# Kernel tuning notes

Measured on AMD Instinct MI355X. Metric: run time of the kernel, lower is better.

Reference implementation:

```python
import jax, jax.numpy as jnp
import numpy as np

EPS = 1e-6
B, N, K = 4, 65536, 16
D_IN, D_OUT, DH = 8, 16, 8  # DH = d_out // 2


def _bn(x, g, b):
    # train-mode BatchNorm2d over (B, N, K) per channel (channels-last here)
    m = jnp.mean(x, axis=(0, 1, 2))
    v = jnp.var(x, axis=(0, 1, 2))
    return (x - m) * jax.lax.rsqrt(v + EPS) * g + b


def _conv(x, w, b):
    # 1x1 Conv2d == per-point linear; x: (B,N,K,Cin), w: (Cout,Cin)
    return jnp.einsum('bnki,oi->bnko', x, w) + b


def _lse(coords, feats, idx, w, b, g, bt):
    # coords: (B,N,3), feats: (B,N,1,D), idx: (B,N,K)
    nbrs = jnp.take_along_axis(coords[:, :, None, :], idx[:, :, :, None], axis=1)  # (B,N,K,3)
    ctr = jnp.broadcast_to(coords[:, :, None, :], nbrs.shape)
    dist = jnp.ones(idx.shape + (1,), dtype=coords.dtype)  # torch path passes idx only -> dist = ones
    enc = jnp.concatenate([ctr, nbrs, ctr - nbrs, dist], axis=-1)  # (B,N,K,10)
    h = jax.nn.relu(_bn(_conv(enc, w, b), g, bt))
    f = jnp.broadcast_to(feats, idx.shape + (feats.shape[-1],))
    return jnp.concatenate([h, f], axis=-1)  # (B,N,K,2*D)


def _pool(x, sw, w, b, g, bt):
    # attentive pooling: softmax over neighbor axis K (axis=2)
    scores = jax.nn.softmax(jnp.einsum('bnki,oi->bnko', x, sw), axis=2)
    agg = jnp.sum(scores * x, axis=2, keepdims=True)  # (B,N,1,C)
    return jax.nn.relu(_bn(_conv(agg, w, b), g, bt))


def setup_inputs() -> dict:
    key = jax.random.key(0)
    ks = jax.random.split(key, 16)
    rn = lambda k, s: (0.1 * jax.random.normal(k, s)).astype(jnp.float32)
    inp = {
        'coords': jax.random.normal(ks[0], (B, N, 3), dtype=jnp.float32),
        'features': jax.random.normal(ks[1], (B, D_IN, N, 1), dtype=jnp.float32),
        'idx': jax.random.randint(ks[2], (B, N, K), 0, N, dtype=jnp.int32),
        # mlp1: d_in -> d_out//2, no bn, LeakyReLU(0.2)
        'w1': rn(ks[3], (DH, D_IN)), 'b1': jnp.zeros((DH,), jnp.float32),
        # lse1 mlp: 10 -> d_out//2, bn + ReLU
        'lse1_w': rn(ks[4], (DH, 10)), 'lse1_b': jnp.zeros((DH,), jnp.float32),
        'lse1_g': jnp.ones((DH,), jnp.float32), 'lse1_bt': jnp.zeros((DH,), jnp.float32),
        # pool1: in d_out -> out d_out//2
        'p1_sw': rn(ks[5], (D_OUT, D_OUT)),
        'p1_w': rn(ks[6], (DH, D_OUT)), 'p1_b': jnp.zeros((DH,), jnp.float32),
        'p1_g': jnp.ones((DH,), jnp.float32), 'p1_bt': jnp.zeros((DH,), jnp.float32),
        # lse2
        'lse2_w': rn(ks[7], (DH, 10)), 'lse2_b': jnp.zeros((DH,), jnp.float32),
        'lse2_g': jnp.ones((DH,), jnp.float32), 'lse2_bt': jnp.zeros((DH,), jnp.float32),
        # pool2: in d_out -> out d_out
        'p2_sw': rn(ks[8], (D_OUT, D_OUT)),
        'p2_w': rn(ks[9], (D_OUT, D_OUT)), 'p2_b': jnp.zeros((D_OUT,), jnp.float32),
        'p2_g': jnp.ones((D_OUT,), jnp.float32), 'p2_bt': jnp.zeros((D_OUT,), jnp.float32),
        # mlp2: d_out -> 2*d_out (no bn/act)
        'w2': rn(ks[10], (2 * D_OUT, D_OUT)), 'b2': jnp.zeros((2 * D_OUT,), jnp.float32),
        # shortcut: d_in -> 2*d_out, bn, no act
        'sc_w': rn(ks[11], (2 * D_OUT, D_IN)), 'sc_b': jnp.zeros((2 * D_OUT,), jnp.float32),
        'sc_g': jnp.ones((2 * D_OUT,), jnp.float32), 'sc_bt': jnp.zeros((2 * D_OUT,), jnp.float32),
    }
    return inp


def reference(coords, features, idx, w1, b1, lse1_w, lse1_b, lse1_g, lse1_bt,
              p1_sw, p1_w, p1_b, p1_g, p1_bt, lse2_w, lse2_b, lse2_g, lse2_bt,
              p2_sw, p2_w, p2_b, p2_g, p2_bt, w2, b2, sc_w, sc_b, sc_g, sc_bt):
    feats = jnp.transpose(features, (0, 2, 3, 1))  # (B,N,1,d_in) channels-last
    x = jax.nn.leaky_relu(_conv(feats, w1, b1), 0.2)           # (B,N,1,DH)
    x = _lse(coords, x, idx, lse1_w, lse1_b, lse1_g, lse1_bt)  # (B,N,K,D_OUT)
    x = _pool(x, p1_sw, p1_w, p1_b, p1_g, p1_bt)               # (B,N,1,DH)
    x = _lse(coords, x, idx, lse2_w, lse2_b, lse2_g, lse2_bt)  # (B,N,K,D_OUT)
    x = _pool(x, p2_sw, p2_w, p2_b, p2_g, p2_bt)               # (B,N,1,D_OUT)
    out = jax.nn.leaky_relu(
        _conv(x, w2, b2) + _bn(_conv(feats, sc_w, sc_b), sc_g, sc_bt), 0.01)
    return jnp.transpose(out, (0, 3, 1, 2))  # (B, 2*d_out, N, 1)
```

## Files before the change

kernel.cpp:

```cpp
#include <hip/hip_runtime.h>

#define NB 4
#define NN 65536
#define NK 16
#define NP (NB * NN)
#define BN_EPS 1e-6f
#define LOG2E 1.44269504088896f

#define WS_ENC_M   0
#define WS_SC_M    32
#define WS_S_Y2    96
#define WS_SS_Y2   104
#define WS_S_Y4    112
#define WS_SS_Y4   128
#define WS_Y2      1024
#define WS_Y4      (1024 + NP * 8)
#define WS_C4      (1024 + NP * 24)

template <int NCH>
__device__ inline void blockReduceAtomic(float (&v)[NCH], float* __restrict__ dst) {
    __shared__ float red[4][NCH];
    const int lane = threadIdx.x & 63;
    const int wv = threadIdx.x >> 6;
    __syncthreads();
#pragma unroll
    for (int c = 0; c < NCH; c++) {
        float x = v[c];
#pragma unroll
        for (int off = 32; off > 0; off >>= 1) x += __shfl_xor(x, off, 64);
        if (lane == 0) red[wv][c] = x;
    }
    __syncthreads();
    for (int c = threadIdx.x; c < NCH; c += 256)
        atomicAdd(dst + c, red[0][c] + red[1][c] + red[2][c] + red[3][c]);
    __syncthreads();
}

__device__ inline void bn_from_enc(const float* __restrict__ M, const float* __restrict__ w,
                                   float b, float g, float bt, float& sc, float& sh) {
    float u[6];
    u[0] = w[0] + w[6]; u[1] = w[1] + w[7]; u[2] = w[2] + w[8];
    u[3] = w[3] - w[6]; u[4] = w[4] - w[7]; u[5] = w[5] - w[8];
    const float beta = b + w[9];
    float lin = 0.f;
#pragma unroll
    for (int i = 0; i < 6; i++) lin += u[i] * M[i];
    float quad = u[0] * u[0] * M[6] + 2.f * u[0] * u[1] * M[7] + 2.f * u[0] * u[2] * M[8]
               + u[1] * u[1] * M[9] + 2.f * u[1] * u[2] * M[10] + u[2] * u[2] * M[11];
#pragma unroll
    for (int i = 0; i < 3; i++)
#pragma unroll
        for (int j = 0; j < 3; j++) quad += 2.f * u[i] * u[3 + j] * M[12 + i * 3 + j];
    quad += u[3] * u[3] * M[21] + 2.f * u[3] * u[4] * M[22] + 2.f * u[3] * u[5] * M[23]
          + u[4] * u[4] * M[24] + 2.f * u[4] * u[5] * M[25] + u[5] * u[5] * M[26];
    const float cnt = (float)NP * (float)NK;
    const float sum = lin + cnt * beta;
    const float ss = quad + 2.f * beta * lin + cnt * beta * beta;
    const float m = sum / cnt, v = ss / cnt - m * m;
    sc = g * rsqrtf(v + BN_EPS);
    sh = bt - m * sc;
}

__global__ __launch_bounds__(256) void k_stats(
    const float* __restrict__ coords, const float* __restrict__ feats,
    const int* __restrict__ idx, float4* __restrict__ c4, float* __restrict__ ws) {
    const int tid = threadIdx.x;
    const int p = blockIdx.x * 256 + tid;
    const int b = p >> 16;
    const int n = p & (NN - 1);

    {
        float accf[44];
        float f[8];
#pragma unroll
        for (int i = 0; i < 8; i++) f[i] = feats[(b * 8 + i) * NN + n];
#pragma unroll
        for (int i = 0; i < 8; i++) accf[i] = f[i];
        int t2 = 8;
#pragma unroll
        for (int i = 0; i < 8; i++)
#pragma unroll
            for (int j = i; j < 8; j++) accf[t2++] = f[i] * f[j];
        blockReduceAtomic<44>(accf, ws + WS_SC_M);
    }

    const float cx = coords[3 * p], cy = coords[3 * p + 1], cz = coords[3 * p + 2];
    c4[p] = make_float4(cx, cy, cz, 0.f);
    const float* cb = coords + b * NN * 3;
    const int4* ip = (const int4*)idx + p * 4;
    float sn0 = 0.f, sn1 = 0.f, sn2 = 0.f;
    float m00 = 0.f, m01 = 0.f, m02 = 0.f, m11 = 0.f, m12 = 0.f, m22 = 0.f;

    auto proc = [&](float nx, float ny, float nz) {
        sn0 += nx; sn1 += ny; sn2 += nz;
        m00 += nx * nx; m01 += nx * ny; m02 += nx * nz;
        m11 += ny * ny; m12 += ny * nz; m22 += nz * nz;
    };

    int4 v0 = ip[0];
    float ax[4], ay[4], az[4];
    {
        int jj[4] = {v0.x, v0.y, v0.z, v0.w};
#pragma unroll
        for (int e = 0; e < 4; e++) {
            ax[e] = cb[3 * jj[e]]; ay[e] = cb[3 * jj[e] + 1]; az[e] = cb[3 * jj[e] + 2];
        }
    }
#pragma unroll 1
    for (int q = 0; q < 3; q++) {
        const int4 vn = ip[q + 1];
        int jj[4] = {vn.x, vn.y, vn.z, vn.w};
        float tx[4], ty[4], tz[4];
#pragma unroll
        for (int e = 0; e < 4; e++) {
            tx[e] = cb[3 * jj[e]]; ty[e] = cb[3 * jj[e] + 1]; tz[e] = cb[3 * jj[e] + 2];
        }
#pragma unroll
        for (int e = 0; e < 4; e++) proc(ax[e], ay[e], az[e]);
#pragma unroll
        for (int e = 0; e < 4; e++) { ax[e] = tx[e]; ay[e] = ty[e]; az[e] = tz[e]; }
    }
#pragma unroll
    for (int e = 0; e < 4; e++) proc(ax[e], ay[e], az[e]);

    float acc[27];
    acc[0] = 16.f * cx; acc[1] = 16.f * cy; acc[2] = 16.f * cz;
    acc[3] = sn0; acc[4] = sn1; acc[5] = sn2;
    acc[6] = 16.f * cx * cx; acc[7] = 16.f * cx * cy; acc[8] = 16.f * cx * cz;
    acc[9] = 16.f * cy * cy; acc[10] = 16.f * cy * cz; acc[11] = 16.f * cz * cz;
    acc[12] = cx * sn0; acc[13] = cx * sn1; acc[14] = cx * sn2;
    acc[15] = cy * sn0; acc[16] = cy * sn1; acc[17] = cy * sn2;
    acc[18] = cz * sn0; acc[19] = cz * sn1; acc[20] = cz * sn2;
    acc[21] = m00; acc[22] = m01; acc[23] = m02;
    acc[24] = m11; acc[25] = m12; acc[26] = m22;
    blockReduceAtomic<27>(acc, ws + WS_ENC_M);
}

__global__ __launch_bounds__(256) void k_pool1(
    const float4* __restrict__ c4, const float* __restrict__ feats,
    const int* __restrict__ idx,
    const float* __restrict__ w1, const float* __restrict__ b1,
    const float* __restrict__ lse1_w, const float* __restrict__ lse1_b,
    const float* __restrict__ lse1_g, const float* __restrict__ lse1_bt,
    const float* __restrict__ lse2_w, const float* __restrict__ lse2_b,
    const float* __restrict__ lse2_g, const float* __restrict__ lse2_bt,
    const float* __restrict__ p1_sw, const float* __restrict__ p1_w,
    const float* __restrict__ p1_b,
    const float* __restrict__ p2_sw, const float* __restrict__ p2_w,
    const float* __restrict__ p2_b, float* __restrict__ ws) {
    __shared__ float an1[24], dcA[24], dkA[8], an2[24], dcB[24], dkB[8],
        sws1[64], sws2[64], pws1[128], pws2[256], pbs1[8], pbs2[16], w1s[64], b1s[8];
    const int tid = threadIdx.x;
    if (tid < 8) {
        const int c = tid;
        {
            const float* w = lse1_w + c * 10;
            float sc, sh;
            bn_from_enc(ws + WS_ENC_M, w, lse1_b[c], lse1_g[c], lse1_bt[c], sc, sh);
#pragma unroll
            for (int i = 0; i < 3; i++) {
                an1[c * 3 + i] = sc * (w[3 + i] - w[6 + i]);
                dcA[c * 3 + i] = sc * (w[i] + w[6 + i]);
            }
            dkA[c] = sc * (lse1_b[c] + w[9]) + sh;
        }
        {
            const float* w = lse2_w + c * 10;
            float sc, sh;
            bn_from_enc(ws + WS_ENC_M, w, lse2_b[c], lse2_g[c], lse2_bt[c], sc, sh);
#pragma unroll
            for (int i = 0; i < 3; i++) {
                an2[c * 3 + i] = sc * (w[3 + i] - w[6 + i]);
                dcB[c * 3 + i] = sc * (w[i] + w[6 + i]);
            }
            dkB[c] = sc * (lse2_b[c] + w[9]) + sh;
        }
        b1s[c] = b1[c]; pbs1[c] = p1_b[c];
    }
    if (tid < 16) pbs2[tid] = p2_b[tid];
    if (tid < 64) {
        w1s[tid] = w1[tid];
        sws1[tid] = p1_sw[(tid >> 3) * 16 + (tid & 7)] * LOG2E;
        sws2[tid] = p2_sw[(tid >> 3) * 16 + (tid & 7)] * LOG2E;
    }
    if (tid < 128) pws1[tid] = p1_w[tid];
    if (tid < 256) pws2[tid] = p2_w[tid];
    __syncthreads();

    const int p = blockIdx.x * 256 + tid;
    const int b = p >> 16;
    const int n = p & (NN - 1);
    const int boff = b << 16;
    const float4 me = c4[p];
    float d1[8], d2[8];
#pragma unroll
    for (int c = 0; c < 8; c++) {
        d1[c] = dcA[c * 3] * me.x + dcA[c * 3 + 1] * me.y + dcA[c * 3 + 2] * me.z + dkA[c];
        d2[c] = dcB[c * 3] * me.x + dcB[c * 3 + 1] * me.y + dcB[c * 3 + 2] * me.z + dkB[c];
    }
    const int4* ip = (const int4*)idx + p * 4;
    float l1[8] = {}, a1[8] = {}, l2[8] = {}, a2[8] = {};

    auto proc = [&](const float4 nn) {
        float h[8];
#pragma unroll
        for (int c = 0; c < 8; c++) {
            float y = an1[c * 3] * nn.x + an1[c * 3 + 1] * nn.y + an1[c * 3 + 2] * nn.z + d1[c];
            h[c] = y > 0.f ? y : 0.f;
        }
#pragma unroll
        for (int o = 0; o < 8; o++) {
            float s = 0.f;
#pragma unroll
            for (int i = 0; i < 8; i++) s += h[i] * sws1[o * 8 + i];
            float e2 = exp2f(s);
            l1[o] += e2; a1[o] += e2 * h[o];
        }
#pragma unroll
        for (int c = 0; c < 8; c++) {
            float y = an2[c * 3] * nn.x + an2[c * 3 + 1] * nn.y + an2[c * 3 + 2] * nn.z + d2[c];
            h[c] = y > 0.f ? y : 0.f;
        }
#pragma unroll
        for (int o = 0; o < 8; o++) {
            float s = 0.f;
#pragma unroll
            for (int i = 0; i < 8; i++) s += h[i] * sws2[o * 8 + i];
            float e2 = exp2f(s);
            l2[o] += e2; a2[o] += e2 * h[o];
        }
    };

    int4 v = ip[0];
    float4 n0 = c4[boff + v.x], n1 = c4[boff + v.y], n2 = c4[boff + v.z], n3 = c4[boff + v.w];
#pragma unroll 1
    for (int q = 0; q < 3; q++) {
        const int4 vn = ip[q + 1];
        const float4 t0 = c4[boff + vn.x], t1 = c4[boff + vn.y],
                     t2 = c4[boff + vn.z], t3 = c4[boff + vn.w];
        proc(n0); proc(n1); proc(n2); proc(n3);
        n0 = t0; n1 = t1; n2 = t2; n3 = t3;
    }
    proc(n0); proc(n1); proc(n2); proc(n3);

    float f[8];
#pragma unroll
    for (int i = 0; i < 8; i++) f[i] = feats[(b * 8 + i) * NN + n];
    float agg[16];
#pragma unroll
    for (int o = 0; o < 8; o++) agg[o] = a1[o] * __builtin_amdgcn_rcpf(l1[o]);
#pragma unroll
    for (int jq = 0; jq < 8; jq++) {
        float y = b1s[jq];
#pragma unroll
        for (int i = 0; i < 8; i++) y += f[i] * w1s[jq * 8 + i];
        agg[8 + jq] = y > 0.f ? y : 0.2f * y;
    }
    float st[16];
#pragma unroll
    for (int c = 0; c < 8; c++) {
        float y = pbs1[c];
#pragma unroll
        for (int o = 0; o < 16; o++) y += agg[o] * pws1[c * 16 + o];
        ws[WS_Y2 + c * NP + p] = y;
        st[c] = y; st[8 + c] = y * y;
    }
    float g2[8];
#pragma unroll
    for (int o = 0; o < 8; o++) g2[o] = a2[o] * __builtin_amdgcn_rcpf(l2[o]);
#pragma unroll
    for (int c = 0; c < 16; c++) {
        float y = pbs2[c];
#pragma unroll
        for (int o = 0; o < 8; o++) y += g2[o] * pws2[c * 16 + o];
        ws[WS_Y4 + c * NP + p] = y;
    }
    blockReduceAtomic<16>(st, ws + WS_S_Y2);
}

__global__ __launch_bounds__(256) void k_pool2e(
    const float* __restrict__ p1_g, const float* __restrict__ p1_bt,
    const float* __restrict__ p2_w, float* __restrict__ ws) {
    __shared__ float p1sc[8], p1sh[8], pwsb[128];
    const int tid = threadIdx.x;
    if (tid < 8) {
        const int c = tid;
        const float cP = 1.f / (float)NP;
        float m = ws[WS_S_Y2 + c] * cP, vv = ws[WS_SS_Y2 + c] * cP - m * m;
        float sc = p1_g[c] * rsqrtf(vv + BN_EPS);
        p1sc[c] = sc; p1sh[c] = p1_bt[c] - m * sc;
    }
    if (tid < 128) pwsb[tid] = p2_w[(tid >> 3) * 16 + 8 + (tid & 7)];
    __syncthreads();

    const int p = blockIdx.x * 256 + tid;
    float x2[8];
#pragma unroll
    for (int c = 0; c < 8; c++) {
        float y = ws[WS_Y2 + c * NP + p] * p1sc[c] + p1sh[c];
        x2[c] = y > 0.f ? y : 0.f;
    }
    float st[32];
#pragma unroll
    for (int c = 0; c < 16; c++) {
        float y = ws[WS_Y4 + c * NP + p];
#pragma unroll
        for (int o = 0; o < 8; o++) y += x2[o] * pwsb[c * 8 + o];
        ws[WS_Y4 + c * NP + p] = y;
        st[c] = y; st[16 + c] = y * y;
    }
    blockReduceAtomic<32>(st, ws + WS_S_Y4);
}

__global__ __launch_bounds__(256) void k_final(
    const float* __restrict__ feats, const float* __restrict__ w2,
    const float* __restrict__ b2, const float* __restrict__ sc_w,
    const float* __restrict__ sc_b, const float* __restrict__ p2_g,
    const float* __restrict__ p2_bt, const float* __restrict__ sc_g,
    const float* __restrict__ sc_bt, const float* __restrict__ ws,
    float* __restrict__ out) {
    __shared__ float w2s[512], b2s[32], scws[256], scbs[32],
        p2sc[16], p2sh[16], scsc[32], scsh[32];
    const int tid = threadIdx.x;
    for (int i = tid; i < 512; i += 256) w2s[i] = w2[i];
    if (tid < 256) scws[tid] = sc_w[tid];
    if (tid < 32) {
        b2s[tid] = b2[tid]; scbs[tid] = sc_b[tid];
        const int c = tid;
        const float* w = sc_w + c * 8;
        const float* S = ws + WS_SC_M;
        float lin = 0.f;
#pragma unroll
        for (int i = 0; i < 8; i++) lin += w[i] * S[i];
        float quad = 0.f;
        int t2 = 0;
#pragma unroll
        for (int i = 0; i < 8; i++)
#pragma unroll
            for (int j = i; j < 8; j++) {
                const float mm = S[8 + t2++];
                quad += (i == j ? 1.f : 2.f) * w[i] * w[j] * mm;
            }
        const float cnt = (float)NP;
        const float bb = sc_b[c];
        const float sum = lin + cnt * bb;
        const float ss = quad + 2.f * bb * lin + cnt * bb * bb;
        const float m = sum / cnt, vv = ss / cnt - m * m;
        const float sc = sc_g[c] * rsqrtf(vv + BN_EPS);
        scsc[c] = sc; scsh[c] = sc_bt[c] - m * sc;
    }
    if (tid < 16) {
        const int c = tid;
        const float cP = 1.f / (float)NP;
        float m = ws[WS_S_Y4 + c] * cP, vv = ws[WS_SS_Y4 + c] * cP - m * m;
        float sc = p2_g[c] * rsqrtf(vv + BN_EPS);
        p2sc[c] = sc; p2sh[c] = p2_bt[c] - m * sc;
    }
    __syncthreads();

    const int p = blockIdx.x * 256 + tid;
    const int b = p >> 16;
    const int n = p & (NN - 1);
    float x4[16];
#pragma unroll
    for (int c = 0; c < 16; c++) {
        float y = ws[WS_Y4 + c * NP + p] * p2sc[c] + p2sh[c];
        x4[c] = y > 0.f ? y : 0.f;
    }
    float f[8];
#pragma unroll
    for (int i = 0; i < 8; i++) f[i] = feats[(b * 8 + i) * NN + n];
#pragma unroll
    for (int c = 0; c < 32; c++) {
        float s = scbs[c];
#pragma unroll
        for (int i = 0; i < 8; i++) s += f[i] * scws[c * 8 + i];
        s = s * scsc[c] + scsh[c];
        float m = b2s[c];
#pragma unroll
        for (int o = 0; o < 16; o++) m += x4[o] * w2s[c * 16 + o];
        float vv = m + s;
        out[(b * 32 + c) * NN + n] = vv > 0.f ? vv : 0.01f * vv;
    }
}

extern "C" void kernel_launch(void* const* d_in, const int* in_sizes, int n_in,
                              void* d_out, int out_size, void* d_ws, size_t ws_size,
                              hipStream_t stream) {
    (void)in_sizes; (void)n_in; (void)out_size; (void)ws_size;
    const float* coords = (const float*)d_in[0];
    const float* features = (const float*)d_in[1];
    const int* idx = (const int*)d_in[2];
    const float* w1 = (const float*)d_in[3];
    const float* b1 = (const float*)d_in[4];
    const float* lse1_w = (const float*)d_in[5];
    const float* lse1_b = (const float*)d_in[6];
    const float* lse1_g = (const float*)d_in[7];
    const float* lse1_bt = (const float*)d_in[8];
    const float* p1_sw = (const float*)d_in[9];
    const float* p1_w = (const float*)d_in[10];
    const float* p1_b = (const float*)d_in[11];
    const float* p1_g = (const float*)d_in[12];
    const float* p1_bt = (const float*)d_in[13];
    const float* lse2_w = (const float*)d_in[14];
    const float* lse2_b = (const float*)d_in[15];
    const float* lse2_g = (const float*)d_in[16];
    const float* lse2_bt = (const float*)d_in[17];
    const float* p2_sw = (const float*)d_in[18];
    const float* p2_w = (const float*)d_in[19];
    const float* p2_b = (const float*)d_in[20];
    const float* p2_g = (const float*)d_in[21];
    const float* p2_bt = (const float*)d_in[22];
    const float* w2 = (const float*)d_in[23];
    const float* b2 = (const float*)d_in[24];
    const float* sc_w = (const float*)d_in[25];
    const float* sc_b = (const float*)d_in[26];
    const float* sc_g = (const float*)d_in[27];
    const float* sc_bt = (const float*)d_in[28];
    float* ws = (float*)d_ws;
    float* out = (float*)d_out;
    float4* c4 = (float4*)(ws + WS_C4);

    const int NBLK = NP / 256;
    (void)hipMemsetAsync(ws, 0, 144 * sizeof(float), stream);
    k_stats<<<NBLK, 256, 0, stream>>>(coords, features, idx, c4, ws);
    k_pool1<<<NBLK, 256, 0, stream>>>(c4, features, idx, w1, b1,
                                      lse1_w, lse1_b, lse1_g, lse1_bt,
                                      lse2_w, lse2_b, lse2_g, lse2_bt,
                                      p1_sw, p1_w, p1_b, p2_sw, p2_w, p2_b, ws);
    k_pool2e<<<NBLK, 256, 0, stream>>>(p1_g, p1_bt, p2_w, ws);
    k_final<<<NBLK, 256, 0, stream>>>(features, w2, b2, sc_w, sc_b, p2_g, p2_bt,
                                      sc_g, sc_bt, ws, out);
}
```

Measured before the change: 335.9 us.

## Materialize gathered neighbor coords in k_stats and stream them in k_pool1

Splits the old stats kernel into a pack kernel (float4 coords plus feature stats) and a stats kernel that gathers neighbors from the packed float4 array. The stats kernel also writes the gathered neighbor coordinates to a coalesced SoA workspace buffer, so k_pool1 reads them with contiguous loads instead of repeating the random idx-based gather. This trades a second random gather for writing and reading about 48 floats per point (roughly 50 MB each way), and adds one kernel launch.

```diff
diff --git a/kernel.cpp b/kernel.cpp
--- a/kernel.cpp
+++ b/kernel.cpp
@@ -16,6 +16,7 @@
 #define WS_Y2      1024
 #define WS_Y4      (1024 + NP * 8)
 #define WS_C4      (1024 + NP * 24)
+#define WS_NB      (1024 + NP * 28)
 
 template <int NCH>
 __device__ inline void blockReduceAtomic(float (&v)[NCH], float* __restrict__ dst) {
@@ -61,76 +62,71 @@
     sh = bt - m * sc;
 }
 
-__global__ __launch_bounds__(256) void k_stats(
+__global__ __launch_bounds__(256) void k_pack(
     const float* __restrict__ coords, const float* __restrict__ feats,
-    const int* __restrict__ idx, float4* __restrict__ c4, float* __restrict__ ws) {
+    float4* __restrict__ c4, float* __restrict__ ws) {
     const int tid = threadIdx.x;
     const int p = blockIdx.x * 256 + tid;
     const int b = p >> 16;
     const int n = p & (NN - 1);
-
-    {
-        float accf[44];
-        float f[8];
-#pragma unroll
-        for (int i = 0; i < 8; i++) f[i] = feats[(b * 8 + i) * NN + n];
-#pragma unroll
-        for (int i = 0; i < 8; i++) accf[i] = f[i];
-        int t2 = 8;
-#pragma unroll
-        for (int i = 0; i < 8; i++)
-#pragma unroll
-            for (int j = i; j < 8; j++) accf[t2++] = f[i] * f[j];
-        blockReduceAtomic<44>(accf, ws + WS_SC_M);
-    }
-
-    const float cx = coords[3 * p], cy = coords[3 * p + 1], cz = coords[3 * p + 2];
-    c4[p] = make_float4(cx, cy, cz, 0.f);
-    const float* cb = coords + b * NN * 3;
+    c4[p] = make_float4(coords[3 * p], coords[3 * p + 1], coords[3 * p + 2], 0.f);
+    float accf[44];
+    float f[8];
+#pragma unroll
+    for (int i = 0; i < 8; i++) f[i] = feats[(b * 8 + i) * NN + n];
+#pragma unroll
+    for (int i = 0; i < 8; i++) accf[i] = f[i];
+    int t2 = 8;
+#pragma unroll
+    for (int i = 0; i < 8; i++)
+#pragma unroll
+        for (int j = i; j < 8; j++) accf[t2++] = f[i] * f[j];
+    blockReduceAtomic<44>(accf, ws + WS_SC_M);
+}
+
+__global__ __launch_bounds__(256) void k_stats(
+    const float4* __restrict__ c4, const int* __restrict__ idx,
+    float* __restrict__ ws) {
+    const int tid = threadIdx.x;
+    const int p = blockIdx.x * 256 + tid;
+    const int b = p >> 16;
+    const int boff = b << 16;
+    float* __restrict__ nbp = ws + WS_NB;
     const int4* ip = (const int4*)idx + p * 4;
+    const float4 me = c4[p];
+
     float sn0 = 0.f, sn1 = 0.f, sn2 = 0.f;
     float m00 = 0.f, m01 = 0.f, m02 = 0.f, m11 = 0.f, m12 = 0.f, m22 = 0.f;
 
-    auto proc = [&](float nx, float ny, float nz) {
-        sn0 += nx; sn1 += ny; sn2 += nz;
-        m00 += nx * nx; m01 += nx * ny; m02 += nx * nz;
-        m11 += ny * ny; m12 += ny * nz; m22 += nz * nz;
+    auto emit = [&](int k, const float4 nn) {
+        nbp[(3 * k    ) * NP + p] = nn.x;
+        nbp[(3 * k + 1) * NP + p] = nn.y;
+        nbp[(3 * k + 2) * NP + p] = nn.z;
+        sn0 += nn.x; sn1 += nn.y; sn2 += nn.z;
+        m00 += nn.x * nn.x; m01 += nn.x * nn.y; m02 += nn.x * nn.z;
+        m11 += nn.y * nn.y; m12 += nn.y * nn.z; m22 += nn.z * nn.z;
     };
 
-    int4 v0 = ip[0];
-    float ax[4], ay[4], az[4];
-    {
-        int jj[4] = {v0.x, v0.y, v0.z, v0.w};
-#pragma unroll
-        for (int e = 0; e < 4; e++) {
-            ax[e] = cb[3 * jj[e]]; ay[e] = cb[3 * jj[e] + 1]; az[e] = cb[3 * jj[e] + 2];
-        }
-    }
+    int4 v = ip[0];
+    float4 n0 = c4[boff + v.x], n1 = c4[boff + v.y], n2 = c4[boff + v.z], n3 = c4[boff + v.w];
 #pragma unroll 1
     for (int q = 0; q < 3; q++) {
         const int4 vn = ip[q + 1];
-        int jj[4] = {vn.x, vn.y, vn.z, vn.w};
-        float tx[4], ty[4], tz[4];
-#pragma unroll
-        for (int e = 0; e < 4; e++) {
-            tx[e] = cb[3 * jj[e]]; ty[e] = cb[3 * jj[e] + 1]; tz[e] = cb[3 * jj[e] + 2];
-        }
-#pragma unroll
-        for (int e = 0; e < 4; e++) proc(ax[e], ay[e], az[e]);
-#pragma unroll
-        for (int e = 0; e < 4; e++) { ax[e] = tx[e]; ay[e] = ty[e]; az[e] = tz[e]; }
-    }
-#pragma unroll
-    for (int e = 0; e < 4; e++) proc(ax[e], ay[e], az[e]);
+        const float4 t0 = c4[boff + vn.x], t1 = c4[boff + vn.y],
+                     t2 = c4[boff + vn.z], t3 = c4[boff + vn.w];
+        emit(4 * q, n0); emit(4 * q + 1, n1); emit(4 * q + 2, n2); emit(4 * q + 3, n3);
+        n0 = t0; n1 = t1; n2 = t2; n3 = t3;
+    }
+    emit(12, n0); emit(13, n1); emit(14, n2); emit(15, n3);
 
     float acc[27];
-    acc[0] = 16.f * cx; acc[1] = 16.f * cy; acc[2] = 16.f * cz;
+    acc[0] = 16.f * me.x; acc[1] = 16.f * me.y; acc[2] = 16.f * me.z;
     acc[3] = sn0; acc[4] = sn1; acc[5] = sn2;
-    acc[6] = 16.f * cx * cx; acc[7] = 16.f * cx * cy; acc[8] = 16.f * cx * cz;
-    acc[9] = 16.f * cy * cy; acc[10] = 16.f * cy * cz; acc[11] = 16.f * cz * cz;
-    acc[12] = cx * sn0; acc[13] = cx * sn1; acc[14] = cx * sn2;
-    acc[15] = cy * sn0; acc[16] = cy * sn1; acc[17] = cy * sn2;
-    acc[18] = cz * sn0; acc[19] = cz * sn1; acc[20] = cz * sn2;
+    acc[6] = 16.f * me.x * me.x; acc[7] = 16.f * me.x * me.y; acc[8] = 16.f * me.x * me.z;
+    acc[9] = 16.f * me.y * me.y; acc[10] = 16.f * me.y * me.z; acc[11] = 16.f * me.z * me.z;
+    acc[12] = me.x * sn0; acc[13] = me.x * sn1; acc[14] = me.x * sn2;
+    acc[15] = me.y * sn0; acc[16] = me.y * sn1; acc[17] = me.y * sn2;
+    acc[18] = me.z * sn0; acc[19] = me.z * sn1; acc[20] = me.z * sn2;
     acc[21] = m00; acc[22] = m01; acc[23] = m02;
     acc[24] = m11; acc[25] = m12; acc[26] = m22;
     blockReduceAtomic<27>(acc, ws + WS_ENC_M);
@@ -138,7 +134,6 @@
 
 __global__ __launch_bounds__(256) void k_pool1(
     const float4* __restrict__ c4, const float* __restrict__ feats,
-    const int* __restrict__ idx,
     const float* __restrict__ w1, const float* __restrict__ b1,
     const float* __restrict__ lse1_w, const float* __restrict__ lse1_b,
     const float* __restrict__ lse1_g, const float* __restrict__ lse1_bt,
@@ -190,7 +185,7 @@
     const int p = blockIdx.x * 256 + tid;
     const int b = p >> 16;
     const int n = p & (NN - 1);
-    const int boff = b << 16;
+    const float* __restrict__ nbp = ws + WS_NB;
     const float4 me = c4[p];
     float d1[8], d2[8];
 #pragma unroll
@@ -198,14 +193,13 @@
         d1[c] = dcA[c * 3] * me.x + dcA[c * 3 + 1] * me.y + dcA[c * 3 + 2] * me.z + dkA[c];
         d2[c] = dcB[c * 3] * me.x + dcB[c * 3 + 1] * me.y + dcB[c * 3 + 2] * me.z + dkB[c];
     }
-    const int4* ip = (const int4*)idx + p * 4;
     float l1[8] = {}, a1[8] = {}, l2[8] = {}, a2[8] = {};
 
-    auto proc = [&](const float4 nn) {
+    auto proc = [&](float nx, float ny, float nz) {
         float h[8];
 #pragma unroll
         for (int c = 0; c < 8; c++) {
-            float y = an1[c * 3] * nn.x + an1[c * 3 + 1] * nn.y + an1[c * 3 + 2] * nn.z + d1[c];
+            float y = an1[c * 3] * nx + an1[c * 3 + 1] * ny + an1[c * 3 + 2] * nz + d1[c];
             h[c] = y > 0.f ? y : 0.f;
         }
 #pragma unroll
@@ -218,7 +212,7 @@
         }
 #pragma unroll
         for (int c = 0; c < 8; c++) {
-            float y = an2[c * 3] * nn.x + an2[c * 3 + 1] * nn.y + an2[c * 3 + 2] * nn.z + d2[c];
+            float y = an2[c * 3] * nx + an2[c * 3 + 1] * ny + an2[c * 3 + 2] * nz + d2[c];
             h[c] = y > 0.f ? y : 0.f;
         }
 #pragma unroll
@@ -231,17 +225,30 @@
         }
     };
 
-    int4 v = ip[0];
-    float4 n0 = c4[boff + v.x], n1 = c4[boff + v.y], n2 = c4[boff + v.z], n3 = c4[boff + v.w];
+    float X[4], Y[4], Z[4];
+#pragma unroll
+    for (int e = 0; e < 4; e++) {
+        X[e] = nbp[(3 * e    ) * NP + p];
+        Y[e] = nbp[(3 * e + 1) * NP + p];
+        Z[e] = nbp[(3 * e + 2) * NP + p];
+    }
 #pragma unroll 1
     for (int q = 0; q < 3; q++) {
-        const int4 vn = ip[q + 1];
-        const float4 t0 = c4[boff + vn.x], t1 = c4[boff + vn.y],
-                     t2 = c4[boff + vn.z], t3 = c4[boff + vn.w];
-        proc(n0); proc(n1); proc(n2); proc(n3);
-        n0 = t0; n1 = t1; n2 = t2; n3 = t3;
-    }
-    proc(n0); proc(n1); proc(n2); proc(n3);
+        float TX[4], TY[4], TZ[4];
+#pragma unroll
+        for (int e = 0; e < 4; e++) {
+            const int k = 4 * (q + 1) + e;
+            TX[e] = nbp[(3 * k    ) * NP + p];
+            TY[e] = nbp[(3 * k + 1) * NP + p];
+            TZ[e] = nbp[(3 * k + 2) * NP + p];
+        }
+#pragma unroll
+        for (int e = 0; e < 4; e++) proc(X[e], Y[e], Z[e]);
+#pragma unroll
+        for (int e = 0; e < 4; e++) { X[e] = TX[e]; Y[e] = TY[e]; Z[e] = TZ[e]; }
+    }
+#pragma unroll
+    for (int e = 0; e < 4; e++) proc(X[e], Y[e], Z[e]);
 
     float f[8];
 #pragma unroll
@@ -423,8 +430,9 @@
 
     const int NBLK = NP / 256;
     (void)hipMemsetAsync(ws, 0, 144 * sizeof(float), stream);
-    k_stats<<<NBLK, 256, 0, stream>>>(coords, features, idx, c4, ws);
-    k_pool1<<<NBLK, 256, 0, stream>>>(c4, features, idx, w1, b1,
+    k_pack<<<NBLK, 256, 0, stream>>>(coords, features, c4, ws);
+    k_stats<<<NBLK, 256, 0, stream>>>(c4, idx, ws);
+    k_pool1<<<NBLK, 256, 0, stream>>>(c4, features, w1, b1,
                                       lse1_w, lse1_b, lse1_g, lse1_bt,
                                       lse2_w, lse2_b, lse2_g, lse2_bt,
                                       p1_sw, p1_w, p1_b, p2_sw, p2_w, p2_b, ws);
```

After: 339.4 us. About the same (+1.0%).
